# Optimization experiments

Hardware: AMD Instinct MI355X
Metric: run time of the kernel (lower is better)

Reference implementation:

```python
import jax, jax.numpy as jnp
import numpy as np

N, E = 50000, 800000
F_IN, H, P, C = 128, 64, 16, 40
L = 3  # gcn_layers


def setup_inputs() -> dict:
    key = jax.random.key(0)
    ks = jax.random.split(key, 10)
    s = 0.05
    return {
        "x_h": jax.random.normal(ks[0], (N, F_IN), jnp.float32),
        "pos_feat": jax.random.normal(ks[1], (N, P), jnp.float32),
        "edge_index": jax.random.randint(ks[2], (2, E), 0, N, dtype=jnp.int32),
        "W_pos": jax.random.normal(ks[3], (P, H), jnp.float32) * s,
        "b_pos": jnp.zeros((H,), jnp.float32),
        "W_init": jax.random.normal(ks[4], (F_IN, H), jnp.float32) * s,
        "b_init": jnp.zeros((H,), jnp.float32),
        "W_l": jax.random.normal(ks[5], (L, H, H), jnp.float32) * s,  # neighbor weight
        "W_r": jax.random.normal(ks[6], (L, H, H), jnp.float32) * s,  # root weight
        "b_conv": jnp.zeros((L, H), jnp.float32),
        "W_last": jax.random.normal(ks[7], (H, C), jnp.float32) * s,
        "b_last": jnp.zeros((C,), jnp.float32),
    }


def _sage_conv(x, src, dst, Wl, Wr, b):
    # PyG SAGEConv(aggr='mean'): out_i = Wl @ mean_{j in N(i)} x_j + Wr @ x_i + b
    msgs = x[src]  # [E, H] gather of source-node features
    agg = jax.ops.segment_sum(msgs, dst, num_segments=N)
    cnt = jax.ops.segment_sum(jnp.ones((E,), x.dtype), dst, num_segments=N)
    agg = agg / jnp.clip(cnt, 1.0, None)[:, None]  # mean; deg-0 nodes -> 0
    return agg @ Wl + x @ Wr + b


def reference(x_h, pos_feat, edge_index, W_pos, b_pos, W_init, b_init,
              W_l, W_r, b_conv, W_last, b_last):
    src, dst = edge_index[0], edge_index[1]
    # pos_embedding -> (hyperbolic encode simplified to identity in Euclidean manifold) -> tanh
    hyp_pos = jnp.tanh(pos_feat @ W_pos + b_pos)  # [N, H]
    h = x_h @ W_init + b_init  # [N, H]
    for i in range(L):
        h = _sage_conv(h, src, dst, W_l[i], W_r[i], b_conv[i])
        if i != L - 1:
            h = h + hyp_pos       # run_base == 'False' branch
            h = jax.nn.relu(h)    # dropout is no-op in eval mode
    emb = h @ W_last + b_last     # [N, C]
    return emb, jax.nn.log_softmax(emb, axis=1)
```

## Files before the change

### kernel.cpp

```cpp
#include <hip/hip_runtime.h>
#include <hip/hip_bf16.h>

#define NN 50000
#define NE 800000
#define FIN 128
#define HD 64
#define NC 40
#define XG   782
#define NB   391
#define NBK  782
#define BW   64

typedef __hip_bfloat16 bf16;
typedef __attribute__((ext_vector_type(8))) short bf16x8;
typedef __attribute__((ext_vector_type(4))) float f32x4;

__device__ __forceinline__ void acc8(float* a, uint4 v){
  a[0] += __uint_as_float(v.x << 16); a[1] += __uint_as_float(v.x & 0xffff0000u);
  a[2] += __uint_as_float(v.y << 16); a[3] += __uint_as_float(v.y & 0xffff0000u);
  a[4] += __uint_as_float(v.z << 16); a[5] += __uint_as_float(v.z & 0xffff0000u);
  a[6] += __uint_as_float(v.w << 16); a[7] += __uint_as_float(v.w & 0xffff0000u);
}

__device__ __forceinline__ unsigned pack2(float lo, float hi){
  union { bf16 b; unsigned short u; } a, b;
  a.b = __float2bfloat16(lo);
  b.b = __float2bfloat16(hi);
  return (unsigned)a.u | ((unsigned)b.u << 16);
}

__device__ __forceinline__ short f2bf_bits(float f){
  union { bf16 b; short s; } u;
  u.b = __float2bfloat16(f);
  return u.s;
}

__device__ __forceinline__ void init_body(
    int wid, const float* __restrict__ x, const float* __restrict__ pos,
    const float* __restrict__ Wi, const float* __restrict__ bi,
    const float* __restrict__ Wp, const float* __restrict__ bp,
    bf16* __restrict__ h0b, bf16* __restrict__ hypb, int lane){
  const int quad = lane >> 4;
  const int col  = lane & 15;
  const int nw   = XG * 4;

  bf16x8 wif[4][4];
  #pragma unroll
  for (int ct = 0; ct < 4; ++ct)
    #pragma unroll
    for (int kf = 0; kf < 4; ++kf)
      #pragma unroll
      for (int j = 0; j < 8; ++j)
        wif[ct][kf][j] = f2bf_bits(Wi[(kf*32 + quad*8 + j)*HD + ct*16 + col]);
  bf16x8 wpf[4];
  #pragma unroll
  for (int ct = 0; ct < 4; ++ct)
    #pragma unroll
    for (int j = 0; j < 8; ++j){
      const int k = quad*8 + j;
      wpf[ct][j] = (k < 16) ? f2bf_bits(Wp[k*HD + ct*16 + col]) : (short)0;
    }
  float bih[4], bph[4];
  #pragma unroll
  for (int c = 0; c < 4; ++c){ bih[c] = bi[c*16 + col]; bph[c] = bp[c*16 + col]; }

  for (int t = wid; t < NN/16; t += nw){
    const int n0 = t * 16;
    bf16x8 af[4];
    #pragma unroll
    for (int kf = 0; kf < 4; ++kf){
      const float* xr = x + (size_t)(n0 + col)*FIN + kf*32 + quad*8;
      const float4 f0 = *(const float4*)xr;
      const float4 f1 = *(const float4*)(xr + 4);
      af[kf][0] = f2bf_bits(f0.x); af[kf][1] = f2bf_bits(f0.y);
      af[kf][2] = f2bf_bits(f0.z); af[kf][3] = f2bf_bits(f0.w);
      af[kf][4] = f2bf_bits(f1.x); af[kf][5] = f2bf_bits(f1.y);
      af[kf][6] = f2bf_bits(f1.z); af[kf][7] = f2bf_bits(f1.w);
    }
    bf16x8 ap;
    #pragma unroll
    for (int j = 0; j < 8; ++j) ap[j] = 0;
    if (quad < 2){
      const float* pr = pos + (size_t)(n0 + col)*16 + quad*8;
      const float4 p0 = *(const float4*)pr;
      const float4 p1 = *(const float4*)(pr + 4);
      ap[0] = f2bf_bits(p0.x); ap[1] = f2bf_bits(p0.y);
      ap[2] = f2bf_bits(p0.z); ap[3] = f2bf_bits(p0.w);
      ap[4] = f2bf_bits(p1.x); ap[5] = f2bf_bits(p1.y);
      ap[6] = f2bf_bits(p1.z); ap[7] = f2bf_bits(p1.w);
    }
    f32x4 ah[4], app[4];
    #pragma unroll
    for (int c = 0; c < 4; ++c){
      ah[c]  = (f32x4){bih[c], bih[c], bih[c], bih[c]};
      app[c] = (f32x4){bph[c], bph[c], bph[c], bph[c]};
    }
    #pragma unroll
    for (int ct = 0; ct < 4; ++ct){
      #pragma unroll
      for (int kf = 0; kf < 4; ++kf)
        ah[ct] = __builtin_amdgcn_mfma_f32_16x16x32_bf16(af[kf], wif[ct][kf], ah[ct], 0, 0, 0);
      app[ct] = __builtin_amdgcn_mfma_f32_16x16x32_bf16(ap, wpf[ct], app[ct], 0, 0, 0);
    }
    #pragma unroll
    for (int reg = 0; reg < 4; ++reg){
      const int n = n0 + quad*4 + reg;
      #pragma unroll
      for (int c = 0; c < 4; ++c){
        h0b[(size_t)n*HD + c*16 + col]  = __float2bfloat16(ah[c][reg]);
        hypb[(size_t)n*HD + c*16 + col] = __float2bfloat16(tanhf(app[c][reg]));
      }
    }
  }
}

__global__ __launch_bounds__(256) void k_hist(
    const int* __restrict__ ei, int* __restrict__ histT,
    const float* __restrict__ x, const float* __restrict__ pos,
    const float* __restrict__ Wi, const float* __restrict__ bi,
    const float* __restrict__ Wp, const float* __restrict__ bp,
    bf16* __restrict__ h0b, bf16* __restrict__ hypb){
  __shared__ int lh[NBK];
  if (blockIdx.x < NB){
    for (int i = threadIdx.x; i < NBK; i += 256) lh[i] = 0;
    __syncthreads();
    int e = blockIdx.x * 2048 + threadIdx.x;
    #pragma unroll
    for (int j = 0; j < 8; ++j, e += 256)
      if (e < NE) atomicAdd(&lh[ei[NE + e] >> 6], 1);
    __syncthreads();
    for (int i = threadIdx.x; i < NBK; i += 256)
      histT[blockIdx.x*NBK + i] = lh[i];
    return;
  }
  init_body((blockIdx.x - NB) * 4 + (threadIdx.x >> 6),
            x, pos, Wi, bi, Wp, bp, h0b, hypb, threadIdx.x & 63);
}

__global__ __launch_bounds__(512) void k_scanA(
    const int* __restrict__ histT, int* __restrict__ ofsT,
    int* __restrict__ totals){
  __shared__ int sc[512];
  const int b = blockIdx.x;
  const int t = threadIdx.x;
  const int v = (t < NB) ? histT[t*NBK + b] : 0;
  sc[t] = v; __syncthreads();
  for (int off = 1; off < 512; off <<= 1){
    const int xv = (t >= off) ? sc[t - off] : 0;
    __syncthreads();
    sc[t] += xv;
    __syncthreads();
  }
  if (t < NB) ofsT[t*NBK + b] = sc[t] - v;
  if (t == 511) totals[b] = sc[511];
}

__global__ __launch_bounds__(1024) void k_scanB(
    const int* __restrict__ totals, int* __restrict__ baseA){
  __shared__ int sc[1024];
  const int t = threadIdx.x;
  const int v = (t < NBK) ? totals[t] : 0;
  sc[t] = v; __syncthreads();
  for (int off = 1; off < 1024; off <<= 1){
    const int xv = (t >= off) ? sc[t - off] : 0;
    __syncthreads();
    sc[t] += xv;
    __syncthreads();
  }
  if (t < NBK) baseA[t] = sc[t] - v;
  if (t == 1023) baseA[NBK] = sc[1023];
}

__global__ __launch_bounds__(256) void k_scatter(
    const int* __restrict__ ei, const int* __restrict__ ofsT,
    const int* __restrict__ baseA, int* __restrict__ packed){
  __shared__ int cur[NBK];
  for (int i = threadIdx.x; i < NBK; i += 256)
    cur[i] = baseA[i] + ofsT[blockIdx.x*NBK + i];
  __syncthreads();
  int e = blockIdx.x * 2048 + threadIdx.x;
  #pragma unroll
  for (int j = 0; j < 8; ++j, e += 256){
    if (e < NE){
      const int d = ei[NE + e];
      const int s = ei[e];
      const int p = atomicAdd(&cur[d >> 6], 1);
      packed[p] = s | ((d & 63) << 16);
    }
  }
}

__global__ __launch_bounds__(256) void k_ell(
    const int* __restrict__ packed, const int* __restrict__ baseA,
    unsigned short* __restrict__ esrc, int* __restrict__ degp){
  __shared__ int cnt[BW];
  __shared__ unsigned short ell[BW * 64];
  if (threadIdx.x < BW) cnt[threadIdx.x] = 0;
  __syncthreads();
  const int b  = blockIdx.x;
  const int lo = baseA[b], hi = baseA[b + 1];
  for (int e = lo + threadIdx.x; e < hi; e += 256){
    const int pk = packed[e];
    const int dl = (pk >> 16) & 63;
    const int p  = atomicAdd(&cnt[dl], 1);
    if (p < 64) ell[dl*64 + p] = (unsigned short)(pk & 0xffff);
  }
  __syncthreads();
  const int n0 = b * BW;
  for (int i = threadIdx.x; i < BW * 8; i += 256){
    const int node = i >> 3;
    if (n0 + node < NN)
      ((uint4*)(esrc + (size_t)(n0 + node)*64))[i & 7] = ((const uint4*)ell)[i];
  }
  for (int i = threadIdx.x; i < BW; i += 256)
    if (n0 + i < NN) degp[n0 + i] = cnt[i];
}

__global__ __launch_bounds__(256) void k_xform(
    const bf16* __restrict__ h, const float* __restrict__ Wl,
    const float* __restrict__ Wr, const float* __restrict__ bc,
    const bf16* __restrict__ hypb, const int use_hyp,
    bf16* __restrict__ y, bf16* __restrict__ z){
  const int lane = threadIdx.x & 63;
  const int quad = lane >> 4;
  const int col  = lane & 15;
  const int wid  = blockIdx.x * 4 + (threadIdx.x >> 6);
  const int nw   = gridDim.x * 4;

  bf16x8 bfr[8][2];
  #pragma unroll
  for (int ct = 0; ct < 8; ++ct){
    const float* W = (ct < 4) ? Wl : Wr;
    const int nc = (ct & 3) * 16 + col;
    #pragma unroll
    for (int kf = 0; kf < 2; ++kf)
      #pragma unroll
      for (int j = 0; j < 8; ++j)
        bfr[ct][kf][j] = f2bf_bits(W[(kf*32 + quad*8 + j)*HD + nc]);
  }
  float zb[4];
  #pragma unroll
  for (int c = 0; c < 4; ++c) zb[c] = bc[c*16 + col];

  for (int t = wid; t < NN/16; t += nw){
    const int n0 = t * 16;
    union { uint4 u; bf16x8 v; } a0, a1;
    a0.u = *(const uint4*)(h + (size_t)(n0 + col)*HD + quad*8);
    a1.u = *(const uint4*)(h + (size_t)(n0 + col)*HD + 32 + quad*8);
    f32x4 acc[8];
    #pragma unroll
    for (int c = 0; c < 4; ++c) acc[c] = (f32x4){0.f, 0.f, 0.f, 0.f};
    #pragma unroll
    for (int c = 0; c < 4; ++c) acc[4+c] = (f32x4){zb[c], zb[c], zb[c], zb[c]};
    #pragma unroll
    for (int ct = 0; ct < 8; ++ct){
      acc[ct] = __builtin_amdgcn_mfma_f32_16x16x32_bf16(a0.v, bfr[ct][0], acc[ct], 0, 0, 0);
      acc[ct] = __builtin_amdgcn_mfma_f32_16x16x32_bf16(a1.v, bfr[ct][1], acc[ct], 0, 0, 0);
    }
    #pragma unroll
    for (int reg = 0; reg < 4; ++reg){
      const int n = n0 + quad*4 + reg;
      #pragma unroll
      for (int c = 0; c < 4; ++c){
        y[(size_t)n*HD + c*16 + col] = __float2bfloat16(acc[c][reg]);
        float zv = acc[4+c][reg];
        if (use_hyp) zv += __bfloat162float(hypb[(size_t)n*HD + c*16 + col]);
        z[(size_t)n*HD + c*16 + col] = __float2bfloat16(zv);
      }
    }
  }
}

__global__ __launch_bounds__(256) void k_gather(
    const bf16* __restrict__ y, const bf16* __restrict__ z,
    const int* __restrict__ degp, const unsigned short* __restrict__ esrc,
    bf16* __restrict__ out, const int do_relu){
  const int lane  = threadIdx.x & 63;
  const int n     = blockIdx.x * 4 + (threadIdx.x >> 6);
  if (n >= NN) return;
  const int fq    = lane & 7;
  const int eslot = lane >> 3;
  const int deg   = min(degp[n], 64);
  const int r0    = n << 6;
  const int r1    = r0 + deg;
  float a0[8] = {0,0,0,0,0,0,0,0};
  float a1[8] = {0,0,0,0,0,0,0,0};
  int e = r0 + eslot;
  for (; e + 8 < r1; e += 16){
    const int s0 = esrc[e];
    const int s1 = esrc[e + 8];
    const uint4 v0 = ((const uint4*)(y + (size_t)s0*HD))[fq];
    const uint4 v1 = ((const uint4*)(y + (size_t)s1*HD))[fq];
    acc8(a0, v0);
    acc8(a1, v1);
  }
  if (e < r1){
    const int s = esrc[e];
    const uint4 v = ((const uint4*)(y + (size_t)s*HD))[fq];
    acc8(a0, v);
  }
  #pragma unroll
  for (int j = 0; j < 8; ++j){
    float s = a0[j] + a1[j];
    s += __shfl_xor(s, 8, 64);
    s += __shfl_xor(s, 16, 64);
    s += __shfl_xor(s, 32, 64);
    a0[j] = s;
  }
  if (eslot == 0){
    const float inv = deg > 0 ? 1.f / (float)deg : 0.f;
    const uint4 zv = ((const uint4*)(z + (size_t)n*HD))[fq];
    float zf[8];
    zf[0] = __uint_as_float(zv.x << 16); zf[1] = __uint_as_float(zv.x & 0xffff0000u);
    zf[2] = __uint_as_float(zv.y << 16); zf[3] = __uint_as_float(zv.y & 0xffff0000u);
    zf[4] = __uint_as_float(zv.z << 16); zf[5] = __uint_as_float(zv.z & 0xffff0000u);
    zf[6] = __uint_as_float(zv.w << 16); zf[7] = __uint_as_float(zv.w & 0xffff0000u);
    float o[8];
    #pragma unroll
    for (int j = 0; j < 8; ++j){
      o[j] = a0[j]*inv + zf[j];
      if (do_relu) o[j] = fmaxf(o[j], 0.f);
    }
    uint4 pv;
    pv.x = pack2(o[0], o[1]);
    pv.y = pack2(o[2], o[3]);
    pv.z = pack2(o[4], o[5]);
    pv.w = pack2(o[6], o[7]);
    ((uint4*)(out + (size_t)n*HD))[fq] = pv;
  }
}

__global__ __launch_bounds__(256) void k_final(
    const bf16* __restrict__ hin, const float* __restrict__ Wl,
    const float* __restrict__ bl, float* __restrict__ out){
  const int lane = threadIdx.x & 63;
  const int quad = lane >> 4;
  const int col  = lane & 15;
  const int wid  = blockIdx.x * 4 + (threadIdx.x >> 6);
  const int nw   = gridDim.x * 4;

  bf16x8 wf[3][2];
  float bb[3];
  #pragma unroll
  for (int ct = 0; ct < 3; ++ct){
    const int nc = ct*16 + col;
    const bool valid = nc < NC;
    bb[ct] = valid ? bl[nc] : -1e30f;
    #pragma unroll
    for (int kf = 0; kf < 2; ++kf)
      #pragma unroll
      for (int j = 0; j < 8; ++j)
        wf[ct][kf][j] = valid ? f2bf_bits(Wl[(kf*32 + quad*8 + j)*NC + nc]) : (short)0;
  }

  for (int t = wid; t < NN/16; t += nw){
    const int n0 = t * 16;
    union { uint4 u; bf16x8 v; } a0, a1;
    a0.u = *(const uint4*)(hin + (size_t)(n0 + col)*HD + quad*8);
    a1.u = *(const uint4*)(hin + (size_t)(n0 + col)*HD + 32 + quad*8);
    f32x4 acc[3];
    #pragma unroll
    for (int ct = 0; ct < 3; ++ct){
      acc[ct] = (f32x4){bb[ct], bb[ct], bb[ct], bb[ct]};
      acc[ct] = __builtin_amdgcn_mfma_f32_16x16x32_bf16(a0.v, wf[ct][0], acc[ct], 0, 0, 0);
      acc[ct] = __builtin_amdgcn_mfma_f32_16x16x32_bf16(a1.v, wf[ct][1], acc[ct], 0, 0, 0);
    }
    #pragma unroll
    for (int reg = 0; reg < 4; ++reg){
      const float e0 = acc[0][reg], e1 = acc[1][reg], e2 = acc[2][reg];
      float vmax = fmaxf(fmaxf(e0, e1), e2);
      vmax = fmaxf(vmax, __shfl_xor(vmax, 1, 64));
      vmax = fmaxf(vmax, __shfl_xor(vmax, 2, 64));
      vmax = fmaxf(vmax, __shfl_xor(vmax, 4, 64));
      vmax = fmaxf(vmax, __shfl_xor(vmax, 8, 64));
      float s = __expf(e0 - vmax) + __expf(e1 - vmax) + __expf(e2 - vmax);
      s += __shfl_xor(s, 1, 64);
      s += __shfl_xor(s, 2, 64);
      s += __shfl_xor(s, 4, 64);
      s += __shfl_xor(s, 8, 64);
      const float off = vmax + __logf(s);
      const int n = n0 + quad*4 + reg;
      #pragma unroll
      for (int ct = 0; ct < 3; ++ct){
        const int nc = ct*16 + col;
        if (nc < NC){
          const float e = acc[ct][reg];
          out[(size_t)n*NC + nc]                 = e;
          out[(size_t)NN*NC + (size_t)n*NC + nc] = e - off;
        }
      }
    }
  }
}

extern "C" void kernel_launch(void* const* d_in, const int* in_sizes, int n_in,
                              void* d_out, int out_size, void* d_ws, size_t ws_size,
                              hipStream_t stream){
  (void)in_sizes; (void)n_in; (void)out_size; (void)ws_size;
  const float* x_h    = (const float*)d_in[0];
  const float* pos    = (const float*)d_in[1];
  const int*   ei     = (const int*)  d_in[2];
  const float* W_pos  = (const float*)d_in[3];
  const float* b_pos  = (const float*)d_in[4];
  const float* W_init = (const float*)d_in[5];
  const float* b_init = (const float*)d_in[6];
  const float* W_l    = (const float*)d_in[7];
  const float* W_r    = (const float*)d_in[8];
  const float* b_conv = (const float*)d_in[9];
  const float* W_last = (const float*)d_in[10];
  const float* b_last = (const float*)d_in[11];
  float* out = (float*)d_out;

  char* p = (char*)d_ws;
  auto alloc = [&](size_t bytes)->char*{
    char* r = p; p += (bytes + 255) & ~(size_t)255; return r;
  };
  bf16* hb0  = (bf16*)alloc((size_t)NN*HD*2);
  bf16* hb1  = (bf16*)alloc((size_t)NN*HD*2);
  bf16* yb   = (bf16*)alloc((size_t)NN*HD*2);
  bf16* zbuf = (bf16*)alloc((size_t)NN*HD*2);
  bf16* hypb = (bf16*)alloc((size_t)NN*HD*2);
  unsigned short* esrc = (unsigned short*)alloc((size_t)NN*64*2);
  int* degp  = (int*)alloc((size_t)NN*4);

  int* histT  = (int*)yb;
  int* ofsT   = histT + NB*NBK;
  int* totals = ofsT + NB*NBK;
  int* baseA  = totals + NBK;
  int* packed = (int*)zbuf;

  k_hist   <<<NB + XG, 256, 0, stream>>>(ei, histT, x_h, pos,
                                         W_init, b_init, W_pos, b_pos, hb0, hypb);
  k_scanA  <<<NBK, 512, 0, stream>>>(histT, ofsT, totals);
  k_scanB  <<<1, 1024, 0, stream>>>(totals, baseA);
  k_scatter<<<NB, 256, 0, stream>>>(ei, ofsT, baseA, packed);
  k_ell    <<<NBK, 256, 0, stream>>>(packed, baseA, esrc, degp);

  bf16* cur = hb0;
  bf16* nxt = hb1;
  for (int l = 0; l < 3; ++l){
    const int last = (l == 2);
    k_xform <<<XG, 256, 0, stream>>>(cur, W_l + l*HD*HD, W_r + l*HD*HD,
                                     b_conv + l*HD, hypb, !last, yb, zbuf);
    k_gather<<<(NN + 3)/4, 256, 0, stream>>>(yb, zbuf, degp, esrc, nxt, !last);
    bf16* t = cur; cur = nxt; nxt = t;
  }
  k_final <<<XG, 256, 0, stream>>>(cur, W_last, b_last, out);
}
```

Before: 261.6 us.

## Map eight nodes per wave in gather, dropping cross-lane reduction

The gather kernel now assigns one 8-lane group per destination node (eight nodes per wavefront) instead of one whole wave per node. Each group loads its edge indices as 16-byte vectors and accumulates neighbor rows serially, which removes the shuffle reduction and the idle lanes in the epilogue. The cost is divergence from varying degrees within a wave, since the loop runs until the largest degree in the wave is covered, and less memory-level parallelism per node.

```diff
diff --git a/kernel.cpp b/kernel.cpp
--- a/kernel.cpp
+++ b/kernel.cpp
@@ -275,59 +275,47 @@
     const bf16* __restrict__ y, const bf16* __restrict__ z,
     const int* __restrict__ degp, const unsigned short* __restrict__ esrc,
     bf16* __restrict__ out, const int do_relu){
-  const int lane  = threadIdx.x & 63;
-  const int n     = blockIdx.x * 4 + (threadIdx.x >> 6);
+  const int lane = threadIdx.x & 63;
+  const int grp  = lane >> 3;
+  const int fq   = lane & 7;
+  const int wave = (blockIdx.x << 2) + (threadIdx.x >> 6);
+  const int n    = (wave << 3) + grp;
   if (n >= NN) return;
-  const int fq    = lane & 7;
-  const int eslot = lane >> 3;
-  const int deg   = min(degp[n], 64);
-  const int r0    = n << 6;
-  const int r1    = r0 + deg;
-  float a0[8] = {0,0,0,0,0,0,0,0};
-  float a1[8] = {0,0,0,0,0,0,0,0};
-  int e = r0 + eslot;
-  for (; e + 8 < r1; e += 16){
-    const int s0 = esrc[e];
-    const int s1 = esrc[e + 8];
-    const uint4 v0 = ((const uint4*)(y + (size_t)s0*HD))[fq];
-    const uint4 v1 = ((const uint4*)(y + (size_t)s1*HD))[fq];
-    acc8(a0, v0);
-    acc8(a1, v1);
-  }
-  if (e < r1){
-    const int s = esrc[e];
-    const uint4 v = ((const uint4*)(y + (size_t)s*HD))[fq];
-    acc8(a0, v);
-  }
+  const int deg = min(degp[n], 64);
+  const uint4* er = (const uint4*)(esrc + ((size_t)n << 6));
+  float a[8] = {0,0,0,0,0,0,0,0};
+  for (int eb = 0; eb < 64; eb += 8){
+    if (!__any(eb < deg)) break;
+    union { uint4 u; unsigned short s[8]; } ev;
+    ev.u = er[eb >> 3];
+    const int m = deg - eb;
+    #pragma unroll
+    for (int j = 0; j < 8; ++j){
+      if (j < m){
+        const uint4 v = ((const uint4*)(y + (size_t)ev.s[j]*HD))[fq];
+        acc8(a, v);
+      }
+    }
+  }
+  const float inv = deg > 0 ? 1.f / (float)deg : 0.f;
+  const uint4 zv = ((const uint4*)(z + (size_t)n*HD))[fq];
+  float zf[8];
+  zf[0] = __uint_as_float(zv.x << 16); zf[1] = __uint_as_float(zv.x & 0xffff0000u);
+  zf[2] = __uint_as_float(zv.y << 16); zf[3] = __uint_as_float(zv.y & 0xffff0000u);
+  zf[4] = __uint_as_float(zv.z << 16); zf[5] = __uint_as_float(zv.z & 0xffff0000u);
+  zf[6] = __uint_as_float(zv.w << 16); zf[7] = __uint_as_float(zv.w & 0xffff0000u);
+  float o[8];
   #pragma unroll
   for (int j = 0; j < 8; ++j){
-    float s = a0[j] + a1[j];
-    s += __shfl_xor(s, 8, 64);
-    s += __shfl_xor(s, 16, 64);
-    s += __shfl_xor(s, 32, 64);
-    a0[j] = s;
-  }
-  if (eslot == 0){
-    const float inv = deg > 0 ? 1.f / (float)deg : 0.f;
-    const uint4 zv = ((const uint4*)(z + (size_t)n*HD))[fq];
-    float zf[8];
-    zf[0] = __uint_as_float(zv.x << 16); zf[1] = __uint_as_float(zv.x & 0xffff0000u);
-    zf[2] = __uint_as_float(zv.y << 16); zf[3] = __uint_as_float(zv.y & 0xffff0000u);
-    zf[4] = __uint_as_float(zv.z << 16); zf[5] = __uint_as_float(zv.z & 0xffff0000u);
-    zf[6] = __uint_as_float(zv.w << 16); zf[7] = __uint_as_float(zv.w & 0xffff0000u);
-    float o[8];
-    #pragma unroll
-    for (int j = 0; j < 8; ++j){
-      o[j] = a0[j]*inv + zf[j];
-      if (do_relu) o[j] = fmaxf(o[j], 0.f);
-    }
-    uint4 pv;
-    pv.x = pack2(o[0], o[1]);
-    pv.y = pack2(o[2], o[3]);
-    pv.z = pack2(o[4], o[5]);
-    pv.w = pack2(o[6], o[7]);
-    ((uint4*)(out + (size_t)n*HD))[fq] = pv;
-  }
+    o[j] = a[j]*inv + zf[j];
+    if (do_relu) o[j] = fmaxf(o[j], 0.f);
+  }
+  uint4 pv;
+  pv.x = pack2(o[0], o[1]);
+  pv.y = pack2(o[2], o[3]);
+  pv.z = pack2(o[4], o[5]);
+  pv.w = pack2(o[6], o[7]);
+  ((uint4*)(out + (size_t)n*HD))[fq] = pv;
 }
 
 __global__ __launch_bounds__(256) void k_final(
@@ -442,7 +430,7 @@
     const int last = (l == 2);
     k_xform <<<XG, 256, 0, stream>>>(cur, W_l + l*HD*HD, W_r + l*HD*HD,
                                      b_conv + l*HD, hypb, !last, yb, zbuf);
-    k_gather<<<(NN + 3)/4, 256, 0, stream>>>(yb, zbuf, degp, esrc, nxt, !last);
+    k_gather<<<1563, 256, 0, stream>>>(yb, zbuf, degp, esrc, nxt, !last);
     bf16* t = cur; cur = nxt; nxt = t;
   }
   k_final <<<XG, 256, 0, stream>>>(cur, W_last, b_last, out);
```

Measured after the change: 253.4 us. 3.1% less time.
